# Kernel tuning notes

Hardware: AMD Instinct MI355X
Metric: run time of the kernel (lower is better)

The kernel has to match this reference:

```python
import jax, jax.numpy as jnp
import numpy as np

TEMP = 0.07
EPS = 1e-6

B = 8192
D1 = 129  # d+1 ambient Lorentz coords


def setup_inputs() -> dict:
    key = jax.random.key(0)
    k1, k2 = jax.random.split(key)
    z1 = jax.random.normal(k1, (B, D1), dtype=jnp.float32)
    z2 = jax.random.normal(k2, (B, D1), dtype=jnp.float32)
    return {"z1": z1, "z2": z2}


def _loss(z1, z2):
    # Minkowski (Lorentz) inner product via a single GEMM:
    # <x,y>_L = -x0*y0 + sum_i xi*yi  ->  x @ (metric * y)^T
    metric = jnp.concatenate([-jnp.ones((1,), z1.dtype), jnp.ones((D1 - 1,), z1.dtype)])
    inner = jnp.einsum('bd,kd->bk', z1, z2 * metric)  # (B, B)
    # Lorentz distance with curvature c=1: acosh(clamp(-<x,y>_L, 1+eps))
    dist = jnp.arccosh(jnp.clip(-inner, 1.0 + EPS, None))
    sims = -dist / TEMP
    # symmetric InfoNCE: labels are the diagonal
    logp_t2i = jax.nn.log_softmax(sims, axis=-1)      # text -> image
    logp_i2t = jax.nn.log_softmax(sims.T, axis=-1)    # image -> text
    diag = jnp.arange(sims.shape[0])
    loss_t2i = -jnp.mean(logp_t2i[diag, diag])
    loss_i2t = -jnp.mean(logp_i2t[diag, diag])
    return (loss_t2i + loss_i2t) / 2.0


def reference(z1, z2):
    return _loss(z1, z2)
```

## Files before the change

kernel.cpp:

```cpp
#include <hip/hip_runtime.h>
#include <math.h>


#define BDIM   8192
#define K_IN   129
#define K_PAD  160
#define BK     32
#define NKT    (K_PAD / BK)
#define CTILES 8

typedef __bf16  bf16x8 __attribute__((ext_vector_type(8)));
typedef float   f32x4  __attribute__((ext_vector_type(4)));

#define OFF_A    0u
#define OFF_B    (BDIM * K_PAD * 2u)
#define OFF_RS   (2u * BDIM * K_PAD * 2u)
#define OFF_CP   (OFF_RS + BDIM * 4u)
#define OFF_DG   (OFF_CP + 4u * BDIM * 4u)

__device__ __forceinline__ float fast_sqrt(float x) {
#if __has_builtin(__builtin_amdgcn_sqrtf)
    return __builtin_amdgcn_sqrtf(x);
#else
    return sqrtf(x);
#endif
}
__device__ __forceinline__ float fast_log2(float x) {
#if __has_builtin(__builtin_amdgcn_logf)
    return __builtin_amdgcn_logf(x);
#else
    return __log2f(x);
#endif
}
__device__ __forceinline__ float fast_exp2(float x) {
#if __has_builtin(__builtin_amdgcn_exp2f)
    return __builtin_amdgcn_exp2f(x);
#else
    extern "C" __device__ float __ocml_native_exp2_f32(float);
    return __ocml_native_exp2_f32(x);
#endif
}

__device__ __forceinline__ unsigned short f2bf_rne(float f) {
    unsigned int u = __float_as_uint(f);
    u += 0x7FFFu + ((u >> 16) & 1u);
    return (unsigned short)(u >> 16);
}

__global__ __launch_bounds__(256) void convert_kernel(
    const float* __restrict__ z1, const float* __restrict__ z2,
    unsigned short* __restrict__ A, unsigned short* __restrict__ B,
    float* __restrict__ rs_cp)
{
    int idx = blockIdx.x * 256 + threadIdx.x;
    if (idx < 5 * BDIM) rs_cp[idx] = 0.f;
    if (idx >= BDIM * K_PAD) return;
    int r = idx / K_PAD;
    int c = idx - r * K_PAD;
    float va = 0.f, vb = 0.f;
    if (c < K_IN) {
        va = z1[r * K_IN + c];
        vb = z2[r * K_IN + c];
        if (c == 0) va = -va;
    }
    A[idx] = f2bf_rne(va);
    B[idx] = f2bf_rne(vb);
}

__global__ __launch_bounds__(256, 3) void gemm_epilogue_kernel(
    const unsigned short* __restrict__ A, const unsigned short* __restrict__ B,
    float* __restrict__ row_sum, float* __restrict__ col_part,
    float* __restrict__ diag)
{
    const int t    = threadIdx.x;
    const int lane = t & 63;
    const int wave = t >> 6;
    const int quad = lane >> 4;
    const int l16  = lane & 15;

    const int strip = blockIdx.x & 63;
    const int chunk = blockIdx.x >> 6;
    const int rowBase  = strip * 128 + wave * 32;
    const int colChunk = chunk * 512;

    const unsigned short* Abase = A + (rowBase + l16) * K_PAD + quad * 8;
    float* colRep = col_part + (strip & 3) * BDIM;

    bf16x8 Ah[2][NKT];
    #pragma unroll
    for (int i = 0; i < 2; ++i)
        #pragma unroll
        for (int kt = 0; kt < NKT; ++kt)
            Ah[i][kt] = *(const bf16x8*)(Abase + i * 16 * K_PAD + kt * BK);

    float rowp[2][4] = {};

    for (int ct = 0; ct < CTILES; ++ct) {
        const int colBase = colChunk + ct * 64;
        const unsigned short* Bbase = B + (colBase + l16) * K_PAD + quad * 8;

        f32x4 acc[2][4] = {};
        #pragma unroll
        for (int kt = 0; kt < NKT; ++kt) {
            bf16x8 bfr[4];
            #pragma unroll
            for (int j = 0; j < 4; ++j)
                bfr[j] = *(const bf16x8*)(Bbase + j * 16 * K_PAD + kt * BK);
            #pragma unroll
            for (int i = 0; i < 2; ++i)
                #pragma unroll
                for (int j = 0; j < 4; ++j)
                    acc[i][j] = __builtin_amdgcn_mfma_f32_16x16x32_bf16(
                                    Ah[i][kt], bfr[j], acc[i][j], 0, 0, 0);
        }

        const bool diagTile = (colBase == (rowBase & ~63));
        const int  dj       = (rowBase >> 4) & 2;
        float colp[4] = {0.f, 0.f, 0.f, 0.f};

        #pragma unroll
        for (int i = 0; i < 2; ++i) {
            #pragma unroll
            for (int j = 0; j < 4; ++j) {
                #pragma unroll
                for (int reg = 0; reg < 4; ++reg) {
                    float inner = acc[i][j][reg];
                    float x = fmaxf(-inner, 1.000001f);
                    float s = fast_sqrt(__builtin_fmaf(x, x, -1.0f));
                    float l2u = fast_log2(x + s);
                    float e = fast_exp2(-14.285714285714286f * l2u);
                    rowp[i][reg] += e;
                    colp[j]      += e;
                    if (diagTile && (j - i) == dj && (quad * 4 + reg) == l16) {
                        int R = rowBase + i * 16 + quad * 4 + reg;
                        diag[R] = -9.902102579427789f * l2u;
                    }
                }
            }
        }

        #pragma unroll
        for (int j = 0; j < 4; ++j) {
            float v = colp[j];
            v += __shfl_xor(v, 16);
            v += __shfl_xor(v, 32);
            if (quad == 0)
                atomicAdd(&colRep[colBase + j * 16 + l16], v);
        }
    }

    #pragma unroll
    for (int i = 0; i < 2; ++i) {
        #pragma unroll
        for (int reg = 0; reg < 4; ++reg) {
            float v = rowp[i][reg];
            v += __shfl_xor(v, 1);
            v += __shfl_xor(v, 2);
            v += __shfl_xor(v, 4);
            v += __shfl_xor(v, 8);
            if (l16 == 0)
                atomicAdd(&row_sum[rowBase + i * 16 + quad * 4 + reg], v);
        }
    }
}

__global__ __launch_bounds__(1024) void finalize_kernel(
    const float* __restrict__ rs, const float* __restrict__ cp,
    const float* __restrict__ dg, float* __restrict__ out)
{
    __shared__ float part[16];
    int t = threadIdx.x;
    float a = 0.f;
    const float LN2_HALF = 0.34657359027997264f;
    for (int b = t; b < BDIM; b += 1024) {
        float cs = cp[b] + cp[b + BDIM] + cp[b + 2 * BDIM] + cp[b + 3 * BDIM];
        a += LN2_HALF * (fast_log2(rs[b]) + fast_log2(cs)) - dg[b];
    }
    #pragma unroll
    for (int m = 1; m < 64; m <<= 1) a += __shfl_xor(a, m);
    if ((t & 63) == 0) part[t >> 6] = a;
    __syncthreads();
    if (t < 16) {
        float v = part[t];
        #pragma unroll
        for (int m = 1; m < 16; m <<= 1) v += __shfl_xor(v, m);
        if (t == 0) out[0] = v * (1.0f / (float)BDIM);
    }
}

extern "C" void kernel_launch(void* const* d_in, const int* in_sizes, int n_in,
                              void* d_out, int out_size, void* d_ws, size_t ws_size,
                              hipStream_t stream)
{
    const float* z1 = (const float*)d_in[0];
    const float* z2 = (const float*)d_in[1];
    float* out = (float*)d_out;

    char* ws = (char*)d_ws;
    unsigned short* A  = (unsigned short*)(ws + OFF_A);
    unsigned short* B  = (unsigned short*)(ws + OFF_B);
    float* row_sum     = (float*)(ws + OFF_RS);
    float* col_part    = (float*)(ws + OFF_CP);
    float* diag        = (float*)(ws + OFF_DG);

    convert_kernel<<<(BDIM * K_PAD + 255) / 256, 256, 0, stream>>>(
        z1, z2, A, B, row_sum );

    gemm_epilogue_kernel<<<1024, 256, 0, stream>>>(
        A, B, row_sum, col_part, diag);

    finalize_kernel<<<1, 1024, 0, stream>>>(row_sum, col_part, diag, out);
}
```

Baseline: 125.0 us.

## Double-buffer B fragments in registers with narrower 32-column tiles

Column tiles in the fused GEMM+epilogue kernel shrink from 64 to 32 columns (doubling the tile count). The B fragments for the next tile are now prefetched into a second register buffer while the current tile's MFMAs and transcendental epilogue run. The aim is to hide global-load latency behind compute. In exchange, the smaller tiles do more column-partial atomics and shuffles per column processed, and the two register buffers raise register pressure under the 3-blocks-per-SM launch bound.

```diff
diff --git a/kernel.cpp b/kernel.cpp
--- a/kernel.cpp
+++ b/kernel.cpp
@@ -7,7 +7,7 @@
 #define K_PAD  160
 #define BK     32
 #define NKT    (K_PAD / BK)
-#define CTILES 8
+#define CTILES 16
 
 typedef __bf16  bf16x8 __attribute__((ext_vector_type(8)));
 typedef float   f32x4  __attribute__((ext_vector_type(4)));
@@ -67,6 +67,62 @@
     B[idx] = f2bf_rne(vb);
 }
 
+
+#define LOADB(buf, cb)                                                       \
+    {                                                                        \
+        const unsigned short* _Bb = B + ((cb) + l16) * K_PAD + quad * 8;     \
+        _Pragma("unroll")                                                    \
+        for (int _j = 0; _j < 2; ++_j)                                       \
+            _Pragma("unroll")                                                \
+            for (int _kt = 0; _kt < NKT; ++_kt)                              \
+                buf[_j * NKT + _kt] =                                        \
+                    *(const bf16x8*)(_Bb + _j * 16 * K_PAD + _kt * BK);      \
+    }
+
+#define COMPUTE(buf, cb)                                                     \
+    {                                                                        \
+        const int colBase = (cb);                                            \
+        f32x4 acc[2][2] = {};                                                \
+        _Pragma("unroll")                                                    \
+        for (int kt = 0; kt < NKT; ++kt)                                     \
+            _Pragma("unroll")                                                \
+            for (int i = 0; i < 2; ++i)                                      \
+                _Pragma("unroll")                                            \
+                for (int j = 0; j < 2; ++j)                                  \
+                    acc[i][j] = __builtin_amdgcn_mfma_f32_16x16x32_bf16(     \
+                        Ah[i][kt], buf[j * NKT + kt], acc[i][j], 0, 0, 0);   \
+        const bool diagTile = (colBase == rowBase);                          \
+        float colp[2] = {0.f, 0.f};                                          \
+        _Pragma("unroll")                                                    \
+        for (int i = 0; i < 2; ++i) {                                        \
+            _Pragma("unroll")                                                \
+            for (int j = 0; j < 2; ++j) {                                    \
+                _Pragma("unroll")                                            \
+                for (int reg = 0; reg < 4; ++reg) {                          \
+                    float inner = acc[i][j][reg];                            \
+                    float x = fmaxf(-inner, 1.000001f);                      \
+                    float s = fast_sqrt(__builtin_fmaf(x, x, -1.0f));        \
+                    float l2u = fast_log2(x + s);                            \
+                    float e = fast_exp2(-14.285714285714286f * l2u);         \
+                    rowp[i][reg] += e;                                       \
+                    colp[j]      += e;                                       \
+                    if (i == j && diagTile && (quad * 4 + reg) == l16) {     \
+                        int R = rowBase + i * 16 + quad * 4 + reg;           \
+                        diag[R] = -9.902102579427789f * l2u;                 \
+                    }                                                        \
+                }                                                            \
+            }                                                                \
+        }                                                                    \
+        _Pragma("unroll")                                                    \
+        for (int j = 0; j < 2; ++j) {                                        \
+            float v = colp[j];                                               \
+            v += __shfl_xor(v, 16);                                          \
+            v += __shfl_xor(v, 32);                                          \
+            if (quad == 0)                                                   \
+                atomicAdd(&colRep[colBase + j * 16 + l16], v);               \
+        }                                                                    \
+    }
+
 __global__ __launch_bounds__(256, 3) void gemm_epilogue_kernel(
     const unsigned short* __restrict__ A, const unsigned short* __restrict__ B,
     float* __restrict__ row_sum, float* __restrict__ col_part,
@@ -95,58 +151,17 @@
 
     float rowp[2][4] = {};
 
-    for (int ct = 0; ct < CTILES; ++ct) {
-        const int colBase = colChunk + ct * 64;
-        const unsigned short* Bbase = B + (colBase + l16) * K_PAD + quad * 8;
-
-        f32x4 acc[2][4] = {};
-        #pragma unroll
-        for (int kt = 0; kt < NKT; ++kt) {
-            bf16x8 bfr[4];
-            #pragma unroll
-            for (int j = 0; j < 4; ++j)
-                bfr[j] = *(const bf16x8*)(Bbase + j * 16 * K_PAD + kt * BK);
-            #pragma unroll
-            for (int i = 0; i < 2; ++i)
-                #pragma unroll
-                for (int j = 0; j < 4; ++j)
-                    acc[i][j] = __builtin_amdgcn_mfma_f32_16x16x32_bf16(
-                                    Ah[i][kt], bfr[j], acc[i][j], 0, 0, 0);
-        }
-
-        const bool diagTile = (colBase == (rowBase & ~63));
-        const int  dj       = (rowBase >> 4) & 2;
-        float colp[4] = {0.f, 0.f, 0.f, 0.f};
-
-        #pragma unroll
-        for (int i = 0; i < 2; ++i) {
-            #pragma unroll
-            for (int j = 0; j < 4; ++j) {
-                #pragma unroll
-                for (int reg = 0; reg < 4; ++reg) {
-                    float inner = acc[i][j][reg];
-                    float x = fmaxf(-inner, 1.000001f);
-                    float s = fast_sqrt(__builtin_fmaf(x, x, -1.0f));
-                    float l2u = fast_log2(x + s);
-                    float e = fast_exp2(-14.285714285714286f * l2u);
-                    rowp[i][reg] += e;
-                    colp[j]      += e;
-                    if (diagTile && (j - i) == dj && (quad * 4 + reg) == l16) {
-                        int R = rowBase + i * 16 + quad * 4 + reg;
-                        diag[R] = -9.902102579427789f * l2u;
-                    }
-                }
-            }
-        }
-
-        #pragma unroll
-        for (int j = 0; j < 4; ++j) {
-            float v = colp[j];
-            v += __shfl_xor(v, 16);
-            v += __shfl_xor(v, 32);
-            if (quad == 0)
-                atomicAdd(&colRep[colBase + j * 16 + l16], v);
-        }
+    bf16x8 bufA[2 * NKT], bufB[2 * NKT];
+    LOADB(bufA, colChunk);
+
+    #pragma unroll 1
+    for (int ct2 = 0; ct2 < CTILES / 2; ++ct2) {
+        const int c0 = colChunk + (ct2 * 2) * 32;
+        LOADB(bufB, c0 + 32);
+        COMPUTE(bufA, c0);
+        if (ct2 < CTILES / 2 - 1)
+            LOADB(bufA, c0 + 64);
+        COMPUTE(bufB, c0 + 32);
     }
 
     #pragma unroll
```

Result: faster. 121.9 us (-2.5%).

## Stage B tiles into double-buffered LDS via async global_load_lds

Applied to the files above, without the earlier changes.

B column tiles are now copied into a two-slot shared-memory buffer with direct global-to-LDS loads. The load for the next tile is issued before the current tile is computed, so global latency can overlap MFMA and epilogue work. All four waves then read one shared copy instead of each fetching B from global memory. The cost is 40KB of LDS per block, which may reduce occupancy below the 3-block launch bound, plus a block barrier per tile. LDS reads of rows with a 320-byte stride may also cause bank conflicts.

```diff
diff --git a/kernel.cpp b/kernel.cpp
--- a/kernel.cpp
+++ b/kernel.cpp
@@ -67,6 +67,73 @@
     B[idx] = f2bf_rne(vb);
 }
 
+
+#define STAGE(bufidx, cb)                                                     \
+    {                                                                         \
+        const char* _gp = (const char*)(B + (size_t)(cb) * K_PAD)             \
+                          + wave * 5120 + lane * 16;                          \
+        unsigned short* _lp = &Bs[bufidx][wave * 2560];                       \
+        _Pragma("unroll")                                                     \
+        for (int _i = 0; _i < 5; ++_i)                                        \
+            __builtin_amdgcn_global_load_lds(                                 \
+                (const __attribute__((address_space(1))) void*)               \
+                    (_gp + _i * 1024),                                        \
+                (__attribute__((address_space(3))) void*)(_lp + _i * 512),    \
+                16, 0, 0);                                                    \
+    }
+
+#define COMPUTE(bufidx, cb)                                                   \
+    {                                                                         \
+        const int colBase = (cb);                                             \
+        const unsigned short* _Bt = &Bs[bufidx][0];                           \
+        f32x4 acc[2][4] = {};                                                 \
+        _Pragma("unroll")                                                     \
+        for (int kt = 0; kt < NKT; ++kt) {                                    \
+            bf16x8 bfr[4];                                                    \
+            _Pragma("unroll")                                                 \
+            for (int j = 0; j < 4; ++j)                                       \
+                bfr[j] = *(const bf16x8*)                                     \
+                    &_Bt[(l16 + j * 16) * K_PAD + quad * 8 + kt * BK];        \
+            _Pragma("unroll")                                                 \
+            for (int i = 0; i < 2; ++i)                                       \
+                _Pragma("unroll")                                             \
+                for (int j = 0; j < 4; ++j)                                   \
+                    acc[i][j] = __builtin_amdgcn_mfma_f32_16x16x32_bf16(      \
+                        Ah[i][kt], bfr[j], acc[i][j], 0, 0, 0);               \
+        }                                                                     \
+        const bool diagTile = (colBase == (rowBase & ~63));                   \
+        const int  dj       = (rowBase >> 4) & 2;                             \
+        float colp[4] = {0.f, 0.f, 0.f, 0.f};                                 \
+        _Pragma("unroll")                                                     \
+        for (int i = 0; i < 2; ++i) {                                         \
+            _Pragma("unroll")                                                 \
+            for (int j = 0; j < 4; ++j) {                                     \
+                _Pragma("unroll")                                             \
+                for (int reg = 0; reg < 4; ++reg) {                           \
+                    float inner = acc[i][j][reg];                             \
+                    float x = fmaxf(-inner, 1.000001f);                       \
+                    float s = fast_sqrt(__builtin_fmaf(x, x, -1.0f));         \
+                    float l2u = fast_log2(x + s);                             \
+                    float e = fast_exp2(-14.285714285714286f * l2u);          \
+                    rowp[i][reg] += e;                                        \
+                    colp[j]      += e;                                        \
+                    if (diagTile && (j - i) == dj && (quad * 4 + reg) == l16){\
+                        int R = rowBase + i * 16 + quad * 4 + reg;            \
+                        diag[R] = -9.902102579427789f * l2u;                  \
+                    }                                                         \
+                }                                                             \
+            }                                                                 \
+        }                                                                     \
+        _Pragma("unroll")                                                     \
+        for (int j = 0; j < 4; ++j) {                                         \
+            float v = colp[j];                                                \
+            v += __shfl_xor(v, 16);                                           \
+            v += __shfl_xor(v, 32);                                           \
+            if (quad == 0)                                                    \
+                atomicAdd(&colRep[colBase + j * 16 + l16], v);                \
+        }                                                                     \
+    }
+
 __global__ __launch_bounds__(256, 3) void gemm_epilogue_kernel(
     const unsigned short* __restrict__ A, const unsigned short* __restrict__ B,
     float* __restrict__ row_sum, float* __restrict__ col_part,
@@ -85,6 +152,8 @@
 
     const unsigned short* Abase = A + (rowBase + l16) * K_PAD + quad * 8;
     float* colRep = col_part + (strip & 3) * BDIM;
+
+    __shared__ __align__(16) unsigned short Bs[2][64 * K_PAD];
 
     bf16x8 Ah[2][NKT];
     #pragma unroll
@@ -95,58 +164,15 @@
 
     float rowp[2][4] = {};
 
+    STAGE(0, colChunk);
+    __syncthreads();
+
+    #pragma unroll 1
     for (int ct = 0; ct < CTILES; ++ct) {
-        const int colBase = colChunk + ct * 64;
-        const unsigned short* Bbase = B + (colBase + l16) * K_PAD + quad * 8;
-
-        f32x4 acc[2][4] = {};
-        #pragma unroll
-        for (int kt = 0; kt < NKT; ++kt) {
-            bf16x8 bfr[4];
-            #pragma unroll
-            for (int j = 0; j < 4; ++j)
-                bfr[j] = *(const bf16x8*)(Bbase + j * 16 * K_PAD + kt * BK);
-            #pragma unroll
-            for (int i = 0; i < 2; ++i)
-                #pragma unroll
-                for (int j = 0; j < 4; ++j)
-                    acc[i][j] = __builtin_amdgcn_mfma_f32_16x16x32_bf16(
-                                    Ah[i][kt], bfr[j], acc[i][j], 0, 0, 0);
-        }
-
-        const bool diagTile = (colBase == (rowBase & ~63));
-        const int  dj       = (rowBase >> 4) & 2;
-        float colp[4] = {0.f, 0.f, 0.f, 0.f};
-
-        #pragma unroll
-        for (int i = 0; i < 2; ++i) {
-            #pragma unroll
-            for (int j = 0; j < 4; ++j) {
-                #pragma unroll
-                for (int reg = 0; reg < 4; ++reg) {
-                    float inner = acc[i][j][reg];
-                    float x = fmaxf(-inner, 1.000001f);
-                    float s = fast_sqrt(__builtin_fmaf(x, x, -1.0f));
-                    float l2u = fast_log2(x + s);
-                    float e = fast_exp2(-14.285714285714286f * l2u);
-                    rowp[i][reg] += e;
-                    colp[j]      += e;
-                    if (diagTile && (j - i) == dj && (quad * 4 + reg) == l16) {
-                        int R = rowBase + i * 16 + quad * 4 + reg;
-                        diag[R] = -9.902102579427789f * l2u;
-                    }
-                }
-            }
-        }
-
-        #pragma unroll
-        for (int j = 0; j < 4; ++j) {
-            float v = colp[j];
-            v += __shfl_xor(v, 16);
-            v += __shfl_xor(v, 32);
-            if (quad == 0)
-                atomicAdd(&colRep[colBase + j * 16 + l16], v);
-        }
+        if (ct + 1 < CTILES)
+            STAGE((ct + 1) & 1, colChunk + (ct + 1) * 64);
+        COMPUTE(ct & 1, colChunk + ct * 64);
+        __syncthreads();
     }
 
     #pragma unroll
```

Measured after the change: 108.8 us. 12.9% less time.
